# Performance work log

Measured on AMD Instinct MI355X. Metric: run time of the kernel, lower is better.

Reference implementation:

```python
import jax, jax.numpy as jnp
import numpy as np

VOCAB, EMB, HID = 120000, 64, 128
B, T = 256, 512


def _rnn_layer(inp, W_ih, b_ih, W_hh, b_hh):
    # inp: [B,T,D]. PyTorch RNN: h_t = tanh(W_ih x_t + b_ih + W_hh h_{t-1} + b_hh)
    pre = jnp.einsum('btd,hd->bth', inp, W_ih) + b_ih + b_hh  # input part hoisted out of scan
    h0 = jnp.zeros((inp.shape[0], W_hh.shape[0]), inp.dtype)

    def step(h, p_t):
        h = jnp.tanh(p_t + h @ W_hh.T)
        return h, h

    hT, outs = jax.lax.scan(step, h0, pre.transpose(1, 0, 2))  # scan over time
    return outs.transpose(1, 0, 2), hT  # [B,T,H], [B,H]


def _layernorm(x, g, b, eps=1e-5):
    mu = jnp.mean(x, axis=-1, keepdims=True)
    var = jnp.var(x, axis=-1, keepdims=True)
    return (x - mu) * jax.lax.rsqrt(var + eps) * g + b


def setup_inputs() -> dict:
    key = jax.random.key(0)
    ks = jax.random.split(key, 10)
    emb = jax.random.normal(ks[0], (VOCAB, EMB), jnp.float32) * 0.02
    emb = emb.at[0].set(0.0)  # padding_idx=0
    s_in, s_h = 1.0 / np.sqrt(HID), 1.0 / np.sqrt(HID)
    return {
        'x': jax.random.randint(ks[1], (B, T), 0, VOCAB),
        'emb': emb,
        'W_ih1': jax.random.normal(ks[2], (HID, EMB), jnp.float32) * s_in,
        'b_ih1': jnp.zeros((HID,), jnp.float32),
        'W_hh1': jax.random.normal(ks[3], (HID, HID), jnp.float32) * s_h,
        'b_hh1': jnp.zeros((HID,), jnp.float32),
        'W_ih2': jax.random.normal(ks[4], (HID, HID), jnp.float32) * s_in,
        'b_ih2': jnp.zeros((HID,), jnp.float32),
        'W_hh2': jax.random.normal(ks[5], (HID, HID), jnp.float32) * s_h,
        'b_hh2': jnp.zeros((HID,), jnp.float32),
        'ln_g': jnp.ones((HID,), jnp.float32),
        'ln_b': jnp.zeros((HID,), jnp.float32),
        'proj_W': jax.random.normal(ks[6], (HID, HID), jnp.float32) * s_h,
        'proj_b': jnp.zeros((HID,), jnp.float32),
        'on_g': jnp.ones((HID,), jnp.float32),
        'on_b': jnp.zeros((HID,), jnp.float32),
    }


def reference(x, emb, W_ih1, b_ih1, W_hh1, b_hh1, W_ih2, b_ih2, W_hh2, b_hh2,
              ln_g, ln_b, proj_W, proj_b, on_g, on_b):
    e = emb[x]                                   # [B,T,64]
    out1, _ = _rnn_layer(e, W_ih1, b_ih1, W_hh1, b_hh1)   # dropout is identity in eval
    _, h2 = _rnn_layer(out1, W_ih2, b_ih2, W_hh2, b_hh2)  # h2: [B,128] (last hidden state)
    rep = _layernorm(h2, ln_g, ln_b)
    rep = jnp.tanh(rep @ proj_W.T + proj_b)
    rep = _layernorm(rep, on_g, on_b)
    return rep
```

## Files before the change

kernel.cpp:

```cpp
#include <hip/hip_runtime.h>

#define HID 128
#define EMB 64
#define VOCAB 120000

__device__ __forceinline__ float fast_tanh(float x) {
    float e = __expf(2.f * x);
    return 1.f - __fdividef(2.f, e + 1.f);
}

#define OPQ(v) asm volatile("" : "+v"(v.x), "+v"(v.y), "+v"(v.z), "+v"(v.w))

#define FMAC(a, h, w) asm("v_fmac_f32 %0, %1, %2" : "+v"(a) : "v"(h), "v"(w))
#define VMUL(a, h, w) asm("v_mul_f32 %0, %1, %2" : "=v"(a) : "v"(h), "v"(w))
#define MAC4(hc, wa, wb, wcc, wd) \
    FMAC(s0, hc, wa); FMAC(s1, hc, wb); FMAC(s2, hc, wcc); FMAC(s3, hc, wd)

#define RED_STAGE(ctrl) \
    "v_add_f32_dpp %0, %0, %0 " ctrl " row_mask:0xf bank_mask:0xf\n\t" \
    "v_add_f32_dpp %1, %1, %1 " ctrl " row_mask:0xf bank_mask:0xf\n\t" \
    "v_add_f32_dpp %2, %2, %2 " ctrl " row_mask:0xf bank_mask:0xf\n\t" \
    "v_add_f32_dpp %3, %3, %3 " ctrl " row_mask:0xf bank_mask:0xf\n\t"
#define REDUCE_L1 asm("s_nop 1\n\t" \
    RED_STAGE("quad_perm:[1,0,3,2]") \
    RED_STAGE("quad_perm:[2,3,0,1]") \
    RED_STAGE("row_half_mirror") \
    : "+v"(s0), "+v"(s1), "+v"(s2), "+v"(s3))
#define REDUCE_L2 asm("s_nop 1\n\t" \
    RED_STAGE("quad_perm:[1,0,3,2]") \
    RED_STAGE("quad_perm:[2,3,0,1]") \
    RED_STAGE("row_half_mirror") \
    RED_STAGE("row_mirror") \
    : "+v"(s0), "+v"(s1), "+v"(s2), "+v"(s3))

__global__ __launch_bounds__(256)
__attribute__((amdgpu_waves_per_eu(1, 2)))
void k_w1e(
    const float* __restrict__ emb, const float* __restrict__ Wih1,
    const float* __restrict__ bih1, const float* __restrict__ bhh1,
    float* __restrict__ W1E)
{
    __shared__ float sA[32][128];
    __shared__ float sW[32][132];
    const int tid = threadIdx.x;
    const int base = blockIdx.x * 128;
    const int tx = tid & 15, ty = tid >> 4;
    const int ox = tx * 8, py = ty * 8;
    const int pl = tid & 127, half = tid >> 7;
    const int rv = min(base + pl, VOCAB - 1);
    float acc[8][8];
#pragma unroll
    for (int p = 0; p < 8; ++p)
#pragma unroll
        for (int o = 0; o < 8; ++o) acc[p][o] = 0.f;
    const float4* ws = (const float4*)(Wih1 + (size_t)pl * EMB + half * 16);
    const float4* as = (const float4*)(emb + (size_t)rv * EMB + half * 16);
    float4 qw[2][4], qe[2][4];
#pragma unroll
    for (int kc = 0; kc < 2; ++kc)
#pragma unroll
        for (int k = 0; k < 4; ++k) {
            qw[kc][k] = ws[kc * 8 + k];
            qe[kc][k] = as[kc * 8 + k];
        }
    for (int kc = 0; kc < 2; ++kc) {
        {
            const int jb = half * 16;
#pragma unroll
            for (int k = 0; k < 4; ++k) {
                float4 q = qw[kc][k], e = qe[kc][k];
                sW[jb + 4*k + 0][pl] = q.x; sW[jb + 4*k + 1][pl] = q.y;
                sW[jb + 4*k + 2][pl] = q.z; sW[jb + 4*k + 3][pl] = q.w;
                sA[jb + 4*k + 0][pl] = e.x; sA[jb + 4*k + 1][pl] = e.y;
                sA[jb + 4*k + 2][pl] = e.z; sA[jb + 4*k + 3][pl] = e.w;
            }
        }
        __syncthreads();
#pragma unroll 4
        for (int j = 0; j < 32; ++j) {
            float4 a0 = *(const float4*)&sA[j][py];
            float4 a1 = *(const float4*)&sA[j][py + 4];
            float4 b0 = *(const float4*)&sW[j][ox];
            float4 b1 = *(const float4*)&sW[j][ox + 4];
            float av[8] = {a0.x,a0.y,a0.z,a0.w,a1.x,a1.y,a1.z,a1.w};
            float bv[8] = {b0.x,b0.y,b0.z,b0.w,b1.x,b1.y,b1.z,b1.w};
#pragma unroll
            for (int p = 0; p < 8; ++p)
#pragma unroll
                for (int o = 0; o < 8; ++o)
                    acc[p][o] = fmaf(av[p], bv[o], acc[p][o]);
        }
        __syncthreads();
    }
    float bo[8];
#pragma unroll
    for (int o = 0; o < 8; ++o) bo[o] = bih1[ox + o] + bhh1[ox + o];
#pragma unroll
    for (int p = 0; p < 8; ++p) {
        const int vout = base + py + p;
        if (vout < VOCAB) {
            float* cp = W1E + (size_t)vout * HID + ox;
            *(float4*)cp       = make_float4(acc[p][0]+bo[0], acc[p][1]+bo[1], acc[p][2]+bo[2], acc[p][3]+bo[3]);
            *(float4*)(cp + 4) = make_float4(acc[p][4]+bo[4], acc[p][5]+bo[5], acc[p][6]+bo[6], acc[p][7]+bo[7]);
        }
    }
}

__device__ inline float bsum768(float v, volatile float* sc, int tid) {
#pragma unroll
    for (int off = 32; off > 0; off >>= 1) v += __shfl_down(v, off, 64);
    __syncthreads();
    if ((tid & 63) == 0) sc[tid >> 6] = v;
    __syncthreads();
    float s = 0.f;
#pragma unroll
    for (int k = 0; k < 12; ++k) s += sc[k];
    return s;
}

__global__ __launch_bounds__(768)
__attribute__((amdgpu_waves_per_eu(3)))
void k_rnn_fused(
    const int* __restrict__ x, const float* __restrict__ W1E,
    const float* __restrict__ Whh1,
    const float* __restrict__ Wih2, const float* __restrict__ bih2,
    const float* __restrict__ bhh2, const float* __restrict__ Whh2,
    const float* __restrict__ ln_g, const float* __restrict__ ln_b,
    const float* __restrict__ projW, const float* __restrict__ proj_b,
    const float* __restrict__ on_g, const float* __restrict__ on_b,
    float* __restrict__ out)
{
    __shared__ __align__(16) float h1[2][160];
    __shared__ __align__(16) float h2[2][160];
    __shared__ int   tok[512];
    __shared__ float sfin[HID];
    __shared__ float xn[HID];
    __shared__ float sc[12];

    const int bb   = blockIdx.x;
    const int tid  = threadIdx.x;
    const int w    = tid >> 6;
    const int lane = tid & 63;
    const bool L1  = (w < 4);
    const int  e   = lane & 7;
    const int  m   = L1 ? 0 : ((lane >> 3) & 1);
    const int  rg  = L1 ? (lane >> 3) : (lane >> 4);
    const int  rowbase = L1 ? (32 * w + rg) : (16 * (w - 4) + rg);
    const int  rstep   = L1 ? 8 : 4;
    const float* wmat  = L1 ? Whh1 : (m ? Whh2 : Wih2);

    const float4* wr0 = (const float4*)(wmat + (size_t)(rowbase            ) * HID + e * 16);
    const float4* wr1 = (const float4*)(wmat + (size_t)(rowbase +     rstep) * HID + e * 16);
    const float4* wr2 = (const float4*)(wmat + (size_t)(rowbase + 2 * rstep) * HID + e * 16);
    const float4* wr3 = (const float4*)(wmat + (size_t)(rowbase + 3 * rstep) * HID + e * 16);
    float4 w0 = wr0[0], w1 = wr0[1], w2  = wr0[2], w3  = wr0[3],
           w4 = wr1[0], w5 = wr1[1], w6  = wr1[2], w7  = wr1[3],
           w8 = wr2[0], w9 = wr2[1], w10 = wr2[2], w11 = wr2[3],
           w12= wr3[0], w13= wr3[1], w14 = wr3[2], w15 = wr3[3];
    OPQ(w0);OPQ(w1);OPQ(w2);OPQ(w3);OPQ(w4);OPQ(w5);OPQ(w6);OPQ(w7);
    OPQ(w8);OPQ(w9);OPQ(w10);OPQ(w11);OPQ(w12);OPQ(w13);OPQ(w14);OPQ(w15);

    const bool wr_en = L1 ? (e < 4) : (m == 0 && e < 4);
    const int  wrow  = rowbase + (e & 3) * rstep;
    const int  wword = ((wrow >> 4) * 20) + (wrow & 15);
    const float b2w  = (!L1 && wr_en) ? (bih2[wrow] + bhh2[wrow]) : 0.f;
    const bool pfe   = L1 && wr_en;

    if (tid < 160) { h1[0][tid] = 0.f; h2[0][tid] = 0.f; }
    if (tid < 512) tok[tid] = x[bb * 512 + tid];

    const float* srcb = (L1 || m == 0) ? &h1[0][0] : &h2[0][0];
    const float4* rp0 = (const float4*)(srcb + e * 20);
    const float4* rp1 = (const float4*)(srcb + 160 + e * 20);
    float* dstb = L1 ? &h1[0][0] : &h2[0][0];
    float* wp_e = dstb + 160 + wword;
    float* wp_o = dstb + wword;

    __syncthreads();

    float pA = 0.f, pB = 0.f;
    if (pfe) {
        pA = W1E[(size_t)tok[0] * HID + wrow];
        pB = W1E[(size_t)tok[1] * HID + wrow];
    }

    auto do_step = [&](int t, float& pslot, int tn, const float4* rp, float* wpt) {
        const float pv = pslot;
        float4 hv0 = rp[0], hv1 = rp[1], hv2 = rp[2], hv3 = rp[3];
        float s0, s1, s2, s3;
        VMUL(s0, hv0.x, w0.x); VMUL(s1, hv0.x, w4.x);
        VMUL(s2, hv0.x, w8.x); VMUL(s3, hv0.x, w12.x);
        MAC4(hv0.y, w0.y, w4.y, w8.y, w12.y);
        MAC4(hv0.z, w0.z, w4.z, w8.z, w12.z);
        MAC4(hv0.w, w0.w, w4.w, w8.w, w12.w);
        MAC4(hv1.x, w1.x, w5.x, w9.x, w13.x);
        MAC4(hv1.y, w1.y, w5.y, w9.y, w13.y);
        MAC4(hv1.z, w1.z, w5.z, w9.z, w13.z);
        MAC4(hv1.w, w1.w, w5.w, w9.w, w13.w);
        MAC4(hv2.x, w2.x, w6.x, w10.x, w14.x);
        MAC4(hv2.y, w2.y, w6.y, w10.y, w14.y);
        MAC4(hv2.z, w2.z, w6.z, w10.z, w14.z);
        MAC4(hv2.w, w2.w, w6.w, w10.w, w14.w);
        MAC4(hv3.x, w3.x, w7.x, w11.x, w15.x);
        MAC4(hv3.y, w3.y, w7.y, w11.y, w15.y);
        MAC4(hv3.z, w3.z, w7.z, w11.z, w15.z);
        MAC4(hv3.w, w3.w, w7.w, w11.w, w15.w);
        if (L1) { REDUCE_L1; } else { REDUCE_L2; }
        if (pfe) pslot = W1E[(size_t)tok[tn] * HID + wrow];
        if (wr_en) {
            float ta = (e & 1) ? s1 : s0;
            float tb = (e & 1) ? s3 : s2;
            float v  = (e & 2) ? tb : ta;
            if (L1) *wpt = fast_tanh(pv + v);
            else    *wpt = (t > 0) ? fast_tanh(b2w + v) : 0.f;
        }
        __syncthreads();
    };

#pragma unroll 1
    for (int t = 0; t < 512; t += 2) {
        do_step(t,     pA, (t + 2 < 512) ? t + 2 : 511, rp0, wp_e);
        do_step(t + 1, pB, (t + 3 < 512) ? t + 3 : 511, rp1, wp_o);
    }

    {
        float* wpD = L1 ? wp_e : &sfin[wrow];
        do_step(512, pA, 511, rp0, wpD);
    }

    const int i = tid & 127;
    float hn = (tid < 128) ? sfin[i] : 0.f;
    float s1v = bsum768(hn, sc, tid);
    float s2v = bsum768(hn * hn, sc, tid);
    float mu = s1v * (1.f / 128.f);
    float var = s2v * (1.f / 128.f) - mu * mu;
    __syncthreads();
    if (tid < 128) xn[i] = (hn - mu) * rsqrtf(var + 1e-5f) * ln_g[i] + ln_b[i];
    __syncthreads();
    float pv = 0.f;
    if (tid < 128) {
        float a0 = proj_b[i], a1 = 0, a2 = 0, a3 = 0;
        const float4* hp = (const float4*)xn;
        const float4* pr = (const float4*)(projW + (size_t)i * HID);
#pragma unroll
        for (int k = 0; k < HID / 4; ++k) {
            float4 u = pr[k];
            float4 hv = hp[k];
            a0 = fmaf(hv.x, u.x, a0); a1 = fmaf(hv.y, u.y, a1);
            a2 = fmaf(hv.z, u.z, a2); a3 = fmaf(hv.w, u.w, a3);
        }
        pv = tanhf((a0 + a1) + (a2 + a3));
    }
    float t1 = bsum768(pv, sc, tid);
    float t2 = bsum768(pv * pv, sc, tid);
    float mu2 = t1 * (1.f / 128.f);
    float var2 = t2 * (1.f / 128.f) - mu2 * mu2;
    if (tid < 128)
        out[(size_t)bb * HID + i] = (pv - mu2) * rsqrtf(var2 + 1e-5f) * on_g[i] + on_b[i];
}

extern "C" void kernel_launch(void* const* d_in, const int* in_sizes, int n_in,
                              void* d_out, int out_size, void* d_ws, size_t ws_size,
                              hipStream_t stream)
{
    const int*   x     = (const int*)  d_in[0];
    const float* emb   = (const float*)d_in[1];
    const float* Wih1  = (const float*)d_in[2];
    const float* bih1  = (const float*)d_in[3];
    const float* Whh1  = (const float*)d_in[4];
    const float* bhh1  = (const float*)d_in[5];
    const float* Wih2  = (const float*)d_in[6];
    const float* bih2  = (const float*)d_in[7];
    const float* Whh2  = (const float*)d_in[8];
    const float* bhh2  = (const float*)d_in[9];
    const float* ln_g  = (const float*)d_in[10];
    const float* ln_b  = (const float*)d_in[11];
    const float* projW = (const float*)d_in[12];
    const float* projb = (const float*)d_in[13];
    const float* on_g  = (const float*)d_in[14];
    const float* on_b  = (const float*)d_in[15];

    float* W1E = (float*)d_ws;

    k_w1e<<<(VOCAB + 127) / 128, 256, 0, stream>>>(emb, Wih1, bih1, bhh1, W1E);
    k_rnn_fused<<<256, 768, 0, stream>>>(x, W1E, Whh1, Wih2, bih2, bhh2, Whh2,
                                         ln_g, ln_b, projW, projb, on_g, on_b,
                                         (float*)d_out);
}
```

Baseline: 433.6 us.

## Compute layer-1 input projection per token in-kernel instead of over whole vocab

Drops the separate kernel that projected the full 120000-row embedding table through W_ih1. Each RNN block now computes the input projection only for its own 512 tokens and stores it as fp16 in about 128KB of dynamic LDS. The per-step global gather of the precomputed projection becomes an LDS read. This removes a large vocabulary-sized GEMM and its global write and read traffic. In exchange it adds a serial prologue inside every block and fp16 rounding of the pre-activations.

```diff
diff --git a/kernel.cpp b/kernel.cpp
--- a/kernel.cpp
+++ b/kernel.cpp
@@ -2,7 +2,7 @@
 
 #define HID 128
 #define EMB 64
-#define VOCAB 120000
+#define SMEM_BYTES 136832
 
 __device__ __forceinline__ float fast_tanh(float x) {
     float e = __expf(2.f * x);
@@ -33,79 +33,6 @@
     RED_STAGE("row_mirror") \
     : "+v"(s0), "+v"(s1), "+v"(s2), "+v"(s3))
 
-__global__ __launch_bounds__(256)
-__attribute__((amdgpu_waves_per_eu(1, 2)))
-void k_w1e(
-    const float* __restrict__ emb, const float* __restrict__ Wih1,
-    const float* __restrict__ bih1, const float* __restrict__ bhh1,
-    float* __restrict__ W1E)
-{
-    __shared__ float sA[32][128];
-    __shared__ float sW[32][132];
-    const int tid = threadIdx.x;
-    const int base = blockIdx.x * 128;
-    const int tx = tid & 15, ty = tid >> 4;
-    const int ox = tx * 8, py = ty * 8;
-    const int pl = tid & 127, half = tid >> 7;
-    const int rv = min(base + pl, VOCAB - 1);
-    float acc[8][8];
-#pragma unroll
-    for (int p = 0; p < 8; ++p)
-#pragma unroll
-        for (int o = 0; o < 8; ++o) acc[p][o] = 0.f;
-    const float4* ws = (const float4*)(Wih1 + (size_t)pl * EMB + half * 16);
-    const float4* as = (const float4*)(emb + (size_t)rv * EMB + half * 16);
-    float4 qw[2][4], qe[2][4];
-#pragma unroll
-    for (int kc = 0; kc < 2; ++kc)
-#pragma unroll
-        for (int k = 0; k < 4; ++k) {
-            qw[kc][k] = ws[kc * 8 + k];
-            qe[kc][k] = as[kc * 8 + k];
-        }
-    for (int kc = 0; kc < 2; ++kc) {
-        {
-            const int jb = half * 16;
-#pragma unroll
-            for (int k = 0; k < 4; ++k) {
-                float4 q = qw[kc][k], e = qe[kc][k];
-                sW[jb + 4*k + 0][pl] = q.x; sW[jb + 4*k + 1][pl] = q.y;
-                sW[jb + 4*k + 2][pl] = q.z; sW[jb + 4*k + 3][pl] = q.w;
-                sA[jb + 4*k + 0][pl] = e.x; sA[jb + 4*k + 1][pl] = e.y;
-                sA[jb + 4*k + 2][pl] = e.z; sA[jb + 4*k + 3][pl] = e.w;
-            }
-        }
-        __syncthreads();
-#pragma unroll 4
-        for (int j = 0; j < 32; ++j) {
-            float4 a0 = *(const float4*)&sA[j][py];
-            float4 a1 = *(const float4*)&sA[j][py + 4];
-            float4 b0 = *(const float4*)&sW[j][ox];
-            float4 b1 = *(const float4*)&sW[j][ox + 4];
-            float av[8] = {a0.x,a0.y,a0.z,a0.w,a1.x,a1.y,a1.z,a1.w};
-            float bv[8] = {b0.x,b0.y,b0.z,b0.w,b1.x,b1.y,b1.z,b1.w};
-#pragma unroll
-            for (int p = 0; p < 8; ++p)
-#pragma unroll
-                for (int o = 0; o < 8; ++o)
-                    acc[p][o] = fmaf(av[p], bv[o], acc[p][o]);
-        }
-        __syncthreads();
-    }
-    float bo[8];
-#pragma unroll
-    for (int o = 0; o < 8; ++o) bo[o] = bih1[ox + o] + bhh1[ox + o];
-#pragma unroll
-    for (int p = 0; p < 8; ++p) {
-        const int vout = base + py + p;
-        if (vout < VOCAB) {
-            float* cp = W1E + (size_t)vout * HID + ox;
-            *(float4*)cp       = make_float4(acc[p][0]+bo[0], acc[p][1]+bo[1], acc[p][2]+bo[2], acc[p][3]+bo[3]);
-            *(float4*)(cp + 4) = make_float4(acc[p][4]+bo[4], acc[p][5]+bo[5], acc[p][6]+bo[6], acc[p][7]+bo[7]);
-        }
-    }
-}
-
 __device__ inline float bsum768(float v, volatile float* sc, int tid) {
 #pragma unroll
     for (int off = 32; off > 0; off >>= 1) v += __shfl_down(v, off, 64);
@@ -121,8 +48,9 @@
 __global__ __launch_bounds__(768)
 __attribute__((amdgpu_waves_per_eu(3)))
 void k_rnn_fused(
-    const int* __restrict__ x, const float* __restrict__ W1E,
-    const float* __restrict__ Whh1,
+    const int* __restrict__ x, const float* __restrict__ emb,
+    const float* __restrict__ Wih1, const float* __restrict__ bih1,
+    const float* __restrict__ bhh1, const float* __restrict__ Whh1,
     const float* __restrict__ Wih2, const float* __restrict__ bih2,
     const float* __restrict__ bhh2, const float* __restrict__ Whh2,
     const float* __restrict__ ln_g, const float* __restrict__ ln_b,
@@ -130,12 +58,14 @@
     const float* __restrict__ on_g, const float* __restrict__ on_b,
     float* __restrict__ out)
 {
-    __shared__ __align__(16) float h1[2][160];
-    __shared__ __align__(16) float h2[2][160];
-    __shared__ int   tok[512];
-    __shared__ float sfin[HID];
-    __shared__ float xn[HID];
-    __shared__ float sc[12];
+    extern __shared__ __align__(16) char smem[];
+    _Float16* spre16 = (_Float16*)smem;
+    float* h1b  = (float*)(smem + 131072);
+    float* h2b  = (float*)(smem + 132352);
+    int*   tok  = (int*)(smem + 133632);
+    float* sfin = (float*)(smem + 135680);
+    float* xn   = (float*)(smem + 136192);
+    float* sc   = (float*)(smem + 136704);
 
     const int bb   = blockIdx.x;
     const int tid  = threadIdx.x;
@@ -149,6 +79,41 @@
     const int  rstep   = L1 ? 8 : 4;
     const float* wmat  = L1 ? Whh1 : (m ? Whh2 : Wih2);
 
+    const bool wr_en = L1 ? (e < 4) : (m == 0 && e < 4);
+    const int  wrow  = rowbase + (e & 3) * rstep;
+    const int  wword = ((wrow >> 4) * 20) + (wrow & 15);
+    const float b2w  = (!L1 && wr_en) ? (bih2[wrow] + bhh2[wrow]) : 0.f;
+    const bool pfe   = L1 && wr_en;
+
+    if (tid < 160) { h1b[tid] = 0.f; h2b[tid] = 0.f; }
+    if (tid < 512) tok[tid] = x[bb * 512 + tid];
+    __syncthreads();
+
+    {
+        const float4* wAp = (const float4*)(Wih1 + (size_t)lane * EMB);
+        const float4* wBp = (const float4*)(Wih1 + (size_t)(lane + 64) * EMB);
+        float4 wa[16], wb[16];
+#pragma unroll
+        for (int k = 0; k < 16; ++k) { wa[k] = wAp[k]; wb[k] = wBp[k]; }
+        const float bA = bih1[lane] + bhh1[lane];
+        const float bB = bih1[lane + 64] + bhh1[lane + 64];
+        for (int t = w; t < 512; t += 12) {
+            const float4* ep = (const float4*)(emb + (size_t)tok[t] * EMB);
+            float a0 = bA, a1 = 0.f, b0 = bB, b1 = 0.f;
+#pragma unroll
+            for (int k = 0; k < 16; ++k) {
+                float4 ev = ep[k];
+                a0 = fmaf(ev.x, wa[k].x, a0); a1 = fmaf(ev.y, wa[k].y, a1);
+                a0 = fmaf(ev.z, wa[k].z, a0); a1 = fmaf(ev.w, wa[k].w, a1);
+                b0 = fmaf(ev.x, wb[k].x, b0); b1 = fmaf(ev.y, wb[k].y, b1);
+                b0 = fmaf(ev.z, wb[k].z, b0); b1 = fmaf(ev.w, wb[k].w, b1);
+            }
+            spre16[t * HID + lane]      = (_Float16)(a0 + a1);
+            spre16[t * HID + lane + 64] = (_Float16)(b0 + b1);
+        }
+    }
+    __syncthreads();
+
     const float4* wr0 = (const float4*)(wmat + (size_t)(rowbase            ) * HID + e * 16);
     const float4* wr1 = (const float4*)(wmat + (size_t)(rowbase +     rstep) * HID + e * 16);
     const float4* wr2 = (const float4*)(wmat + (size_t)(rowbase + 2 * rstep) * HID + e * 16);
@@ -160,28 +125,17 @@
     OPQ(w0);OPQ(w1);OPQ(w2);OPQ(w3);OPQ(w4);OPQ(w5);OPQ(w6);OPQ(w7);
     OPQ(w8);OPQ(w9);OPQ(w10);OPQ(w11);OPQ(w12);OPQ(w13);OPQ(w14);OPQ(w15);
 
-    const bool wr_en = L1 ? (e < 4) : (m == 0 && e < 4);
-    const int  wrow  = rowbase + (e & 3) * rstep;
-    const int  wword = ((wrow >> 4) * 20) + (wrow & 15);
-    const float b2w  = (!L1 && wr_en) ? (bih2[wrow] + bhh2[wrow]) : 0.f;
-    const bool pfe   = L1 && wr_en;
-
-    if (tid < 160) { h1[0][tid] = 0.f; h2[0][tid] = 0.f; }
-    if (tid < 512) tok[tid] = x[bb * 512 + tid];
-
-    const float* srcb = (L1 || m == 0) ? &h1[0][0] : &h2[0][0];
+    const float* srcb = (L1 || m == 0) ? h1b : h2b;
     const float4* rp0 = (const float4*)(srcb + e * 20);
     const float4* rp1 = (const float4*)(srcb + 160 + e * 20);
-    float* dstb = L1 ? &h1[0][0] : &h2[0][0];
+    float* dstb = L1 ? h1b : h2b;
     float* wp_e = dstb + 160 + wword;
     float* wp_o = dstb + wword;
 
-    __syncthreads();
-
     float pA = 0.f, pB = 0.f;
     if (pfe) {
-        pA = W1E[(size_t)tok[0] * HID + wrow];
-        pB = W1E[(size_t)tok[1] * HID + wrow];
+        pA = (float)spre16[wrow];
+        pB = (float)spre16[HID + wrow];
     }
 
     auto do_step = [&](int t, float& pslot, int tn, const float4* rp, float* wpt) {
@@ -206,7 +160,7 @@
         MAC4(hv3.z, w3.z, w7.z, w11.z, w15.z);
         MAC4(hv3.w, w3.w, w7.w, w11.w, w15.w);
         if (L1) { REDUCE_L1; } else { REDUCE_L2; }
-        if (pfe) pslot = W1E[(size_t)tok[tn] * HID + wrow];
+        if (pfe) pslot = (float)spre16[tn * HID + wrow];
         if (wr_en) {
             float ta = (e & 1) ? s1 : s0;
             float tb = (e & 1) ? s3 : s2;
@@ -280,10 +234,10 @@
     const float* on_g  = (const float*)d_in[14];
     const float* on_b  = (const float*)d_in[15];
 
-    float* W1E = (float*)d_ws;
-
-    k_w1e<<<(VOCAB + 127) / 128, 256, 0, stream>>>(emb, Wih1, bih1, bhh1, W1E);
-    k_rnn_fused<<<256, 768, 0, stream>>>(x, W1E, Whh1, Wih2, bih2, bhh2, Whh2,
-                                         ln_g, ln_b, projW, projb, on_g, on_b,
-                                         (float*)d_out);
-}
+    hipFuncSetAttribute(reinterpret_cast<const void*>(k_rnn_fused),
+                        hipFuncAttributeMaxDynamicSharedMemorySize, SMEM_BYTES);
+
+    k_rnn_fused<<<256, 768, SMEM_BYTES, stream>>>(
+        x, emb, Wih1, bih1, bhh1, Whh1, Wih2, bih2, bhh2, Whh2,
+        ln_g, ln_b, projW, projb, on_g, on_b, (float*)d_out);
+}
```

Measured after the change: 1.031 ms. +137.8%, slower.
